# Kernel optimization log

Measured on AMD Instinct MI355X. Metric: run time of the kernel, lower is better.

## Reference

```python
import jax, jax.numpy as jnp
import numpy as np

N_NODES = 100000
N_EDGES = 1600000
IN, HID, OUT = 128, 128, 64


def setup_inputs() -> dict:
    key = jax.random.key(0)
    ks = jax.random.split(key, 12)
    x = jax.random.normal(ks[0], (N_NODES, IN), dtype=jnp.float32)
    src = jax.random.randint(ks[1], (N_EDGES,), 0, N_NODES, dtype=jnp.int32)
    dst = jax.random.randint(ks[2], (N_EDGES,), 0, N_NODES, dtype=jnp.int32)
    def lin(k, fan_in, fan_out):
        s = 1.0 / np.sqrt(fan_in)
        return (jax.random.normal(k, (fan_in, fan_out), dtype=jnp.float32) * s)
    dims = [(IN, HID), (HID, HID), (HID, OUT)]
    params = {}
    for l, (fi, fo) in enumerate(dims):
        params[f"Wself{l}"] = lin(ks[3 + 3 * l], fi, fo)
        params[f"Wneigh{l}"] = lin(ks[4 + 3 * l], fi, fo)
        params[f"b{l}"] = jnp.zeros((fo,), dtype=jnp.float32)
    return {"x": x, "src": src, "dst": dst, **params}


def _sage_conv(h, src, dst, inv_deg, Ws, Wn, b):
    # mean aggregation over in-neighbors: segment-sum of gathered src feats / degree
    agg = jax.ops.segment_sum(h[src], dst, num_segments=N_NODES) * inv_deg
    return h @ Ws + agg @ Wn + b


def reference(x, src, dst, Wself0, Wneigh0, b0, Wself1, Wneigh1, b1, Wself2, Wneigh2, b2):
    deg = jax.ops.segment_sum(jnp.ones((N_EDGES,), jnp.float32), dst, num_segments=N_NODES)
    inv_deg = (1.0 / jnp.maximum(deg, 1.0))[:, None]  # zero-degree nodes get zero agg
    h = jax.nn.relu(_sage_conv(x, src, dst, inv_deg, Wself0, Wneigh0, b0))
    h = jax.nn.relu(_sage_conv(h, src, dst, inv_deg, Wself1, Wneigh1, b1))
    h = _sage_conv(h, src, dst, inv_deg, Wself2, Wneigh2, b2)
    return h
```

## Files before the change

kernel.cpp:

```cpp
#include <hip/hip_runtime.h>
#include <hip/hip_bf16.h>

#define N_NODES 100000
#define N_EDGES 1600000
#define BSHIFT 8
#define NB 391
#define BCAP 8192

typedef __attribute__((ext_vector_type(8))) short short8;
typedef __attribute__((ext_vector_type(4))) float f32x4;
typedef unsigned short ushort;
typedef unsigned int uint;

__device__ __forceinline__ ushort f2bf(float f) {
    uint u = __float_as_uint(f);
    uint r = (u + 0x7fffu + ((u >> 16) & 1u)) >> 16;
    return (ushort)r;
}
__device__ __forceinline__ float bflo(uint v) { return __uint_as_float(v << 16); }
__device__ __forceinline__ float bfhi(uint v) { return __uint_as_float(v & 0xffff0000u); }


__global__ __launch_bounds__(256) void partA_kernel(const int* __restrict__ src,
                                                    const int* __restrict__ dst,
                                                    uint* __restrict__ packed,
                                                    int* __restrict__ bucket_cnt, int E) {
    constexpr int PER = 16;
    __shared__ int cnt[NB];
    __shared__ int cur[NB];
    int tid = threadIdx.x;
    for (int i = tid; i < NB; i += 256) cnt[i] = 0;
    __syncthreads();
    int base = blockIdx.x * (256 * PER);
    int d[PER], s[PER];
#pragma unroll
    for (int i = 0; i < PER; i++) {
        int e = base + tid + i * 256;
        if (e < E) {
            d[i] = dst[e];
            s[i] = src[e];
            atomicAdd(&cnt[d[i] >> BSHIFT], 1);
        } else {
            d[i] = -1;
        }
    }
    __syncthreads();
    for (int i = tid; i < NB; i += 256) cur[i] = atomicAdd(&bucket_cnt[i], cnt[i]);
    __syncthreads();
#pragma unroll
    for (int i = 0; i < PER; i++) {
        if (d[i] >= 0) {
            int b = d[i] >> BSHIFT;
            int p = atomicAdd(&cur[b], 1);
            packed[(size_t)b * BCAP + p] = ((uint)(d[i] & 255) << 17) | (uint)s[i];
        }
    }
}


#define KE 20

__global__ __launch_bounds__(256) void partB_kernel(const uint* __restrict__ packed,
                                                    const int* __restrict__ bucket_cnt,
                                                    int* __restrict__ row_ptr,
                                                    float* __restrict__ inv_deg,
                                                    int* __restrict__ col, int N, int E) {
    __shared__ int deg[256];
    __shared__ int cur[256];
    __shared__ int psum[256];
    __shared__ int sofs;
    int b = blockIdx.x, tid = threadIdx.x;
    int cnt = bucket_cnt[b];
    {
        int part = 0;
        for (int i = tid; i < b; i += 256) part += bucket_cnt[i];
        psum[tid] = part;
        __syncthreads();
        for (int off = 128; off > 0; off >>= 1) {
            if (tid < off) psum[tid] += psum[tid + off];
            __syncthreads();
        }
        if (tid == 0) sofs = psum[0];
        __syncthreads();
    }
    int bofs = sofs;
    const uint* pk = packed + (size_t)b * BCAP;
    deg[tid] = 0;
    __syncthreads();
    uint w[KE];
#pragma unroll
    for (int j = 0; j < KE; j++) {
        int ee = tid + j * 256;
        if (ee < cnt) {
            w[j] = pk[ee];
            atomicAdd(&deg[w[j] >> 17], 1);
        }
    }
    for (int ee = tid + KE * 256; ee < cnt; ee += 256)
        atomicAdd(&deg[pk[ee] >> 17], 1);
    __syncthreads();
    int d0 = deg[tid];
    psum[tid] = d0;
    __syncthreads();
    for (int off = 1; off < 256; off <<= 1) {
        int x = psum[tid];
        int y = (tid >= off) ? psum[tid - off] : 0;
        __syncthreads();
        psum[tid] = x + y;
        __syncthreads();
    }
    int excl = psum[tid] - d0;
    cur[tid] = excl;
    int g = (b << BSHIFT) + tid;
    if (g < N) {
        row_ptr[g] = bofs + excl;
        inv_deg[g] = 1.0f / (float)(d0 > 1 ? d0 : 1);
    }
    if (b == 0 && tid == 0) row_ptr[N] = E;
    __syncthreads();
#pragma unroll
    for (int j = 0; j < KE; j++) {
        int ee = tid + j * 256;
        if (ee < cnt) {
            int p = atomicAdd(&cur[w[j] >> 17], 1);
            col[bofs + p] = (int)(w[j] & 0x1FFFFu);
        }
    }
    for (int ee = tid + KE * 256; ee < cnt; ee += 256) {
        uint ww = pk[ee];
        int p = atomicAdd(&cur[ww >> 17], 1);
        col[bofs + p] = (int)(ww & 0x1FFFFu);
    }
}


#define CAST_BLK 6250

__global__ __launch_bounds__(256) void prep_kernel(const float* __restrict__ x,
                                                   ushort* __restrict__ xb,
                                                   const float* __restrict__ Ws0,
                                                   const float* __restrict__ Wn0,
                                                   const float* __restrict__ Ws1,
                                                   const float* __restrict__ Wn1,
                                                   const float* __restrict__ Ws2,
                                                   const float* __restrict__ Wn2,
                                                   ushort* __restrict__ BT0,
                                                   ushort* __restrict__ BT1,
                                                   ushort* __restrict__ BT2) {
    int blk = blockIdx.x;
    if (blk < CAST_BLK) {
        long n8 = (long)N_NODES * 128 / 8;
        long g = (long)blk * 256 + threadIdx.x;
        if (g >= n8) return;
        const float4* x4 = (const float4*)x;
        float4 a = x4[g * 2], b = x4[g * 2 + 1];
        uint4 o;
        o.x = (uint)f2bf(a.x) | ((uint)f2bf(a.y) << 16);
        o.y = (uint)f2bf(a.z) | ((uint)f2bf(a.w) << 16);
        o.z = (uint)f2bf(b.x) | ((uint)f2bf(b.y) << 16);
        o.w = (uint)f2bf(b.z) | ((uint)f2bf(b.w) << 16);
        ((uint4*)xb)[g] = o;
        return;
    }
    int idx = (blk - CAST_BLK) * 256 + threadIdx.x;
    const float* Ws;
    const float* Wn;
    ushort* BT;
    int FOUT;
    if (idx < 128 * 256) {
        Ws = Ws0; Wn = Wn0; BT = BT0; FOUT = 128;
    } else if (idx < 2 * 128 * 256) {
        idx -= 128 * 256;
        Ws = Ws1; Wn = Wn1; BT = BT1; FOUT = 128;
    } else if (idx < 2 * 128 * 256 + 64 * 256) {
        idx -= 2 * 128 * 256;
        Ws = Ws2; Wn = Wn2; BT = BT2; FOUT = 64;
    } else {
        return;
    }
    int n = idx >> 8, k = idx & 255;
    float v = (k < 128) ? Ws[k * FOUT + n] : Wn[(k - 128) * FOUT + n];
    BT[idx] = f2bf(v);
}


#define ASTR 136

template <int FOUT, bool RELU, bool OUTBF16>
__global__ __launch_bounds__(256) void fused_layer(const ushort* __restrict__ hb,
                                                   const int* __restrict__ row_ptr,
                                                   const int* __restrict__ col,
                                                   const float* __restrict__ inv_deg,
                                                   const ushort* __restrict__ BTb,
                                                   const float* __restrict__ bias,
                                                   void* __restrict__ outp, int nNodes) {
    constexpr int NT = FOUT / 16;
    constexpr int BSTR = 40;
    __shared__ ushort BT[FOUT * BSTR];
    __shared__ ushort AGG[64 * ASTR];
    int tid = threadIdx.x;
    int wave = tid >> 6, lane = tid & 63;
    int quad = lane >> 4, sub = lane & 15;
    int suboff = sub * 16;
    const char* hbase = (const char*)hb;
    int r0 = blockIdx.x * 64 + wave * 16;

    for (int i = 0; i < 16; i++) {
        int node = r0 + i;
        if (node >= nNodes) node = nNodes - 1;
        int beg = row_ptr[node], end = row_ptr[node + 1];
        float acc[8];
#pragma unroll
        for (int j = 0; j < 8; j++) acc[j] = 0.f;
        for (int e0 = beg; e0 < end; e0 += 16) {
            int rem = end - e0;
            int idxv[4];
            float msk[4];
#pragma unroll
            for (int j = 0; j < 4; j++) {
                int ii = quad + 4 * j;
                msk[j] = (ii < rem) ? 1.f : 0.f;
                idxv[j] = col[e0 + ((ii < rem) ? ii : 0)];
            }
            uint4 v[4];
#pragma unroll
            for (int j = 0; j < 4; j++)
                v[j] = *(const uint4*)(hbase + (((uint)idxv[j] << 8) + suboff));
#pragma unroll
            for (int j = 0; j < 4; j++) {
                acc[0] += bflo(v[j].x) * msk[j]; acc[1] += bfhi(v[j].x) * msk[j];
                acc[2] += bflo(v[j].y) * msk[j]; acc[3] += bfhi(v[j].y) * msk[j];
                acc[4] += bflo(v[j].z) * msk[j]; acc[5] += bfhi(v[j].z) * msk[j];
                acc[6] += bflo(v[j].w) * msk[j]; acc[7] += bfhi(v[j].w) * msk[j];
            }
        }
#pragma unroll
        for (int j = 0; j < 8; j++) {
            acc[j] += __shfl_xor(acc[j], 16);
            acc[j] += __shfl_xor(acc[j], 32);
        }
        if (quad == 0) {
            float inv = inv_deg[node];
            uint4 o;
            o.x = (uint)f2bf(acc[0] * inv) | ((uint)f2bf(acc[1] * inv) << 16);
            o.y = (uint)f2bf(acc[2] * inv) | ((uint)f2bf(acc[3] * inv) << 16);
            o.z = (uint)f2bf(acc[4] * inv) | ((uint)f2bf(acc[5] * inv) << 16);
            o.w = (uint)f2bf(acc[6] * inv) | ((uint)f2bf(acc[7] * inv) << 16);
            *(uint4*)&AGG[(wave * 16 + i) * ASTR + sub * 8] = o;
        }
    }
    __syncthreads();

    int m = lane & 15;
    int arow = r0 + m;
    if (arow >= nNodes) arow = nNodes - 1;
    const ushort* hrow = hb + (size_t)arow * 128;

    f32x4 acc[NT];
#pragma unroll
    for (int t = 0; t < NT; t++) acc[t] = (f32x4){0.f, 0.f, 0.f, 0.f};

#pragma unroll
    for (int kc = 0; kc < 8; kc++) {
        __syncthreads();
        constexpr int UNITS = FOUT * 4;
#pragma unroll
        for (int u0 = 0; u0 < UNITS / 256; u0++) {
            int u = tid + u0 * 256;
            int n = u >> 2, ko = (u & 3) * 8;
            short8 v = *(const short8*)(BTb + n * 256 + kc * 32 + ko);
            *(short8*)(&BT[n * BSTR + ko]) = v;
        }
        __syncthreads();
        short8 afrag;
        if (kc < 4) {
            afrag = *(const short8*)(hrow + kc * 32 + quad * 8);
        } else {
            afrag = *(const short8*)(&AGG[(wave * 16 + m) * ASTR + (kc - 4) * 32 + quad * 8]);
        }
#pragma unroll
        for (int t = 0; t < NT; t++) {
            short8 bfrag = *(const short8*)(&BT[(t * 16 + m) * BSTR + quad * 8]);
            acc[t] = __builtin_amdgcn_mfma_f32_16x16x32_bf16(afrag, bfrag, acc[t], 0, 0, 0);
        }
    }

#pragma unroll
    for (int reg = 0; reg < 4; reg++) {
        int orow = r0 + quad * 4 + reg;
        if (orow < nNodes) {
#pragma unroll
            for (int t = 0; t < NT; t++) {
                int j = t * 16 + m;
                float v = acc[t][reg] + bias[j];
                if (RELU) v = fmaxf(v, 0.f);
                if (OUTBF16)
                    ((ushort*)outp)[(size_t)orow * FOUT + j] = f2bf(v);
                else
                    ((float*)outp)[(size_t)orow * FOUT + j] = v;
            }
        }
    }
}

extern "C" void kernel_launch(void* const* d_in, const int* in_sizes, int n_in,
                              void* d_out, int out_size, void* d_ws, size_t ws_size,
                              hipStream_t stream) {
    const float* x   = (const float*)d_in[0];
    const int* src   = (const int*)d_in[1];
    const int* dst   = (const int*)d_in[2];
    const float* Ws0 = (const float*)d_in[3];
    const float* Wn0 = (const float*)d_in[4];
    const float* b0  = (const float*)d_in[5];
    const float* Ws1 = (const float*)d_in[6];
    const float* Wn1 = (const float*)d_in[7];
    const float* b1  = (const float*)d_in[8];
    const float* Ws2 = (const float*)d_in[9];
    const float* Wn2 = (const float*)d_in[10];
    const float* b2  = (const float*)d_in[11];
    float* out = (float*)d_out;

    const int N = N_NODES, E = N_EDGES;

    char* p = (char*)d_ws;
    auto take = [&](size_t bytes) {
        void* r = (void*)p;
        p += (bytes + 255) & ~(size_t)255;
        return r;
    };
    uint* packed    = (uint*)take((size_t)NB * BCAP * 4);
    int* bucket_cnt = (int*)take((size_t)NB * 4);
    int* row_ptr    = (int*)take((size_t)(N + 1) * 4);
    int* col        = (int*)take((size_t)E * 4);
    float* inv_deg  = (float*)take((size_t)N * 4);
    ushort* xb      = (ushort*)take((size_t)N * 128 * 2);
    ushort* h1b     = (ushort*)take((size_t)N * 128 * 2);
    ushort* BT0     = (ushort*)take((size_t)128 * 256 * 2);
    ushort* BT1     = (ushort*)take((size_t)128 * 256 * 2);
    ushort* BT2     = (ushort*)take((size_t)64 * 256 * 2);

    hipMemsetAsync(bucket_cnt, 0, (size_t)NB * 4, stream);
    int nblkA = (E + 4096 - 1) / 4096;
    partA_kernel<<<nblkA, 256, 0, stream>>>(src, dst, packed, bucket_cnt, E);
    partB_kernel<<<NB, 256, 0, stream>>>(packed, bucket_cnt, row_ptr, inv_deg, col, N, E);

    prep_kernel<<<CAST_BLK + 320, 256, 0, stream>>>(x, xb, Ws0, Wn0, Ws1, Wn1, Ws2, Wn2,
                                                    BT0, BT1, BT2);

    int grid = (N + 63) / 64;

    fused_layer<128, true, true><<<grid, 256, 0, stream>>>(xb, row_ptr, col, inv_deg,
                                                           BT0, b0, h1b, N);
    fused_layer<128, true, true><<<grid, 256, 0, stream>>>(h1b, row_ptr, col, inv_deg,
                                                           BT1, b1, xb, N);
    fused_layer<64, false, false><<<grid, 256, 0, stream>>>(xb, row_ptr, col, inv_deg,
                                                            BT2, b2, out, N);
}
```

Before: 420.4 us.

## Split aggregation from GEMM, transform-then-aggregate last layer, fuse prep with partition

The fused per-layer kernel is split into a one-node-per-wave aggregation kernel and a separate MFMA GEMM that computes 32 rows per wave. The last layer now applies the weights before aggregating, so it gathers 64-wide projected features instead of 128-wide inputs. Edge partitioning, input casting and weight transposition are merged into one launch, and partitioning uses per-wave shared counters to reduce atomic contention. In exchange, the aggregated features make an extra round trip through global memory, and there are more kernel launches.

```diff
diff --git a/kernel.cpp b/kernel.cpp
--- a/kernel.cpp
+++ b/kernel.cpp
@@ -21,39 +21,95 @@
 __device__ __forceinline__ float bfhi(uint v) { return __uint_as_float(v & 0xffff0000u); }
 
 
-__global__ __launch_bounds__(256) void partA_kernel(const int* __restrict__ src,
-                                                    const int* __restrict__ dst,
-                                                    uint* __restrict__ packed,
-                                                    int* __restrict__ bucket_cnt, int E) {
-    constexpr int PER = 16;
-    __shared__ int cnt[NB];
-    __shared__ int cur[NB];
+#define CAST_BLK 6250
+#define PREP_BLK (CAST_BLK + 128 + 128 + 64)
+
+__global__ __launch_bounds__(256) void fusedA_kernel(const int* __restrict__ src,
+                                                     const int* __restrict__ dst,
+                                                     uint* __restrict__ packed,
+                                                     int* __restrict__ bucket_cnt, int E,
+                                                     const float* __restrict__ x,
+                                                     ushort* __restrict__ xb,
+                                                     const float* __restrict__ Ws0,
+                                                     const float* __restrict__ Wn0,
+                                                     const float* __restrict__ Ws1,
+                                                     const float* __restrict__ Wn1,
+                                                     const float* __restrict__ Ws2,
+                                                     const float* __restrict__ Wn2,
+                                                     ushort* __restrict__ BT0,
+                                                     ushort* __restrict__ BT1,
+                                                     ushort* __restrict__ BT2) {
+    __shared__ int cnt4[4][NB];
+    __shared__ int cur4[4][NB];
     int tid = threadIdx.x;
-    for (int i = tid; i < NB; i += 256) cnt[i] = 0;
-    __syncthreads();
-    int base = blockIdx.x * (256 * PER);
-    int d[PER], s[PER];
-#pragma unroll
-    for (int i = 0; i < PER; i++) {
-        int e = base + tid + i * 256;
-        if (e < E) {
-            d[i] = dst[e];
-            s[i] = src[e];
-            atomicAdd(&cnt[d[i] >> BSHIFT], 1);
-        } else {
-            d[i] = -1;
-        }
-    }
-    __syncthreads();
-    for (int i = tid; i < NB; i += 256) cur[i] = atomicAdd(&bucket_cnt[i], cnt[i]);
-    __syncthreads();
-#pragma unroll
-    for (int i = 0; i < PER; i++) {
-        if (d[i] >= 0) {
-            int b = d[i] >> BSHIFT;
-            int p = atomicAdd(&cur[b], 1);
-            packed[(size_t)b * BCAP + p] = ((uint)(d[i] & 255) << 17) | (uint)s[i];
-        }
+    if (blockIdx.x < NB) {
+        constexpr int PER = 16;
+        int w = tid >> 6;
+        for (int i = tid; i < 4 * NB; i += 256) ((int*)cnt4)[i] = 0;
+        __syncthreads();
+        int base = blockIdx.x * (256 * PER);
+        int d[PER], s[PER];
+#pragma unroll
+        for (int i = 0; i < PER; i++) {
+            int e = base + tid + i * 256;
+            if (e < E) {
+                d[i] = dst[e];
+                s[i] = src[e];
+                atomicAdd(&cnt4[w][d[i] >> BSHIFT], 1);
+            } else {
+                d[i] = -1;
+            }
+        }
+        __syncthreads();
+        for (int i = tid; i < NB; i += 256) {
+            int c0 = cnt4[0][i], c1 = cnt4[1][i], c2 = cnt4[2][i], c3 = cnt4[3][i];
+            int b0 = atomicAdd(&bucket_cnt[i], c0 + c1 + c2 + c3);
+            cur4[0][i] = b0;
+            cur4[1][i] = b0 + c0;
+            cur4[2][i] = b0 + c0 + c1;
+            cur4[3][i] = b0 + c0 + c1 + c2;
+        }
+        __syncthreads();
+#pragma unroll
+        for (int i = 0; i < PER; i++) {
+            if (d[i] >= 0) {
+                int b = d[i] >> BSHIFT;
+                int p = atomicAdd(&cur4[w][b], 1);
+                packed[(size_t)b * BCAP + p] = ((uint)(d[i] & 255) << 17) | (uint)s[i];
+            }
+        }
+        return;
+    }
+    int blk = blockIdx.x - NB;
+    if (blk < CAST_BLK) {
+        long n8 = (long)N_NODES * 128 / 8;
+        long g = (long)blk * 256 + tid;
+        if (g >= n8) return;
+        const float4* x4 = (const float4*)x;
+        float4 a = x4[g * 2], b = x4[g * 2 + 1];
+        uint4 o;
+        o.x = (uint)f2bf(a.x) | ((uint)f2bf(a.y) << 16);
+        o.y = (uint)f2bf(a.z) | ((uint)f2bf(a.w) << 16);
+        o.z = (uint)f2bf(b.x) | ((uint)f2bf(b.y) << 16);
+        o.w = (uint)f2bf(b.z) | ((uint)f2bf(b.w) << 16);
+        ((uint4*)xb)[g] = o;
+        return;
+    }
+    int idx = (blk - CAST_BLK) * 256 + tid;
+    if (idx < 128 * 256) {
+        int n = idx >> 8, k = idx & 255;
+        float v = (k < 128) ? Ws0[k * 128 + n] : Wn0[(k - 128) * 128 + n];
+        BT0[idx] = f2bf(v);
+    } else if (idx < 2 * 128 * 256) {
+        idx -= 128 * 256;
+        int n = idx >> 8, k = idx & 255;
+        float v = (k < 128) ? Ws1[k * 128 + n] : Wn1[(k - 128) * 128 + n];
+        BT1[idx] = f2bf(v);
+    } else if (idx < 2 * 128 * 256 + 128 * 128) {
+        idx -= 2 * 128 * 256;
+        int n = idx >> 7, k = idx & 127;
+        float v = (n < 64) ? Ws2[k * 64 + n] : Wn2[k * 64 + (n - 64)];
+        BT2[idx] = f2bf(v);
     }
 }
 
@@ -134,131 +190,86 @@
 }
 
 
-#define CAST_BLK 6250
-
-__global__ __launch_bounds__(256) void prep_kernel(const float* __restrict__ x,
-                                                   ushort* __restrict__ xb,
-                                                   const float* __restrict__ Ws0,
-                                                   const float* __restrict__ Wn0,
-                                                   const float* __restrict__ Ws1,
-                                                   const float* __restrict__ Wn1,
-                                                   const float* __restrict__ Ws2,
-                                                   const float* __restrict__ Wn2,
-                                                   ushort* __restrict__ BT0,
-                                                   ushort* __restrict__ BT1,
-                                                   ushort* __restrict__ BT2) {
-    int blk = blockIdx.x;
-    if (blk < CAST_BLK) {
-        long n8 = (long)N_NODES * 128 / 8;
-        long g = (long)blk * 256 + threadIdx.x;
-        if (g >= n8) return;
-        const float4* x4 = (const float4*)x;
-        float4 a = x4[g * 2], b = x4[g * 2 + 1];
+__global__ __launch_bounds__(256) void agg_kernel(const ushort* __restrict__ hb,
+                                                  const int* __restrict__ row_ptr,
+                                                  const int* __restrict__ col,
+                                                  const float* __restrict__ inv_deg,
+                                                  ushort* __restrict__ aggb, int n) {
+    int node = (int)((blockIdx.x * blockDim.x + threadIdx.x) >> 6);
+    int lane = threadIdx.x & 63;
+    if (node >= n) return;
+    int quad = lane >> 4;
+    int sub = lane & 15;
+    const char* hbase = (const char*)hb;
+    int beg = row_ptr[node], end = row_ptr[node + 1];
+    float acc[8];
+#pragma unroll
+    for (int j = 0; j < 8; j++) acc[j] = 0.f;
+    int suboff = sub * 16;
+    for (int e0 = beg; e0 < end; e0 += 16) {
+        int rem = end - e0;
+        int idxv[4];
+        float msk[4];
+#pragma unroll
+        for (int j = 0; j < 4; j++) {
+            int i = quad + 4 * j;
+            msk[j] = (i < rem) ? 1.f : 0.f;
+            idxv[j] = col[e0 + ((i < rem) ? i : 0)];
+        }
+        uint4 v[4];
+#pragma unroll
+        for (int j = 0; j < 4; j++)
+            v[j] = *(const uint4*)(hbase + (((uint)idxv[j] << 8) + suboff));
+#pragma unroll
+        for (int j = 0; j < 4; j++) {
+            acc[0] += bflo(v[j].x) * msk[j]; acc[1] += bfhi(v[j].x) * msk[j];
+            acc[2] += bflo(v[j].y) * msk[j]; acc[3] += bfhi(v[j].y) * msk[j];
+            acc[4] += bflo(v[j].z) * msk[j]; acc[5] += bfhi(v[j].z) * msk[j];
+            acc[6] += bflo(v[j].w) * msk[j]; acc[7] += bfhi(v[j].w) * msk[j];
+        }
+    }
+#pragma unroll
+    for (int j = 0; j < 8; j++) {
+        acc[j] += __shfl_xor(acc[j], 16);
+        acc[j] += __shfl_xor(acc[j], 32);
+    }
+    if (quad == 0) {
+        float inv = inv_deg[node];
         uint4 o;
-        o.x = (uint)f2bf(a.x) | ((uint)f2bf(a.y) << 16);
-        o.y = (uint)f2bf(a.z) | ((uint)f2bf(a.w) << 16);
-        o.z = (uint)f2bf(b.x) | ((uint)f2bf(b.y) << 16);
-        o.w = (uint)f2bf(b.z) | ((uint)f2bf(b.w) << 16);
-        ((uint4*)xb)[g] = o;
-        return;
-    }
-    int idx = (blk - CAST_BLK) * 256 + threadIdx.x;
-    const float* Ws;
-    const float* Wn;
-    ushort* BT;
-    int FOUT;
-    if (idx < 128 * 256) {
-        Ws = Ws0; Wn = Wn0; BT = BT0; FOUT = 128;
-    } else if (idx < 2 * 128 * 256) {
-        idx -= 128 * 256;
-        Ws = Ws1; Wn = Wn1; BT = BT1; FOUT = 128;
-    } else if (idx < 2 * 128 * 256 + 64 * 256) {
-        idx -= 2 * 128 * 256;
-        Ws = Ws2; Wn = Wn2; BT = BT2; FOUT = 64;
-    } else {
-        return;
-    }
-    int n = idx >> 8, k = idx & 255;
-    float v = (k < 128) ? Ws[k * FOUT + n] : Wn[(k - 128) * FOUT + n];
-    BT[idx] = f2bf(v);
-}
-
-
-#define ASTR 136
-
-template <int FOUT, bool RELU, bool OUTBF16>
-__global__ __launch_bounds__(256) void fused_layer(const ushort* __restrict__ hb,
-                                                   const int* __restrict__ row_ptr,
-                                                   const int* __restrict__ col,
-                                                   const float* __restrict__ inv_deg,
-                                                   const ushort* __restrict__ BTb,
-                                                   const float* __restrict__ bias,
-                                                   void* __restrict__ outp, int nNodes) {
+        o.x = (uint)f2bf(acc[0] * inv) | ((uint)f2bf(acc[1] * inv) << 16);
+        o.y = (uint)f2bf(acc[2] * inv) | ((uint)f2bf(acc[3] * inv) << 16);
+        o.z = (uint)f2bf(acc[4] * inv) | ((uint)f2bf(acc[5] * inv) << 16);
+        o.w = (uint)f2bf(acc[6] * inv) | ((uint)f2bf(acc[7] * inv) << 16);
+        *(uint4*)((char*)aggb + (size_t)node * 256 + suboff) = o;
+    }
+}
+
+
+template <int FOUT, bool RELU>
+__global__ __launch_bounds__(256) void mfma_gemm(const ushort* __restrict__ hb,
+                                                 const ushort* __restrict__ aggb,
+                                                 const ushort* __restrict__ BTb,
+                                                 const float* __restrict__ bias,
+                                                 ushort* __restrict__ outp, int nNodes) {
     constexpr int NT = FOUT / 16;
     constexpr int BSTR = 40;
     __shared__ ushort BT[FOUT * BSTR];
-    __shared__ ushort AGG[64 * ASTR];
     int tid = threadIdx.x;
     int wave = tid >> 6, lane = tid & 63;
-    int quad = lane >> 4, sub = lane & 15;
-    int suboff = sub * 16;
-    const char* hbase = (const char*)hb;
-    int r0 = blockIdx.x * 64 + wave * 16;
-
-    for (int i = 0; i < 16; i++) {
-        int node = r0 + i;
-        if (node >= nNodes) node = nNodes - 1;
-        int beg = row_ptr[node], end = row_ptr[node + 1];
-        float acc[8];
-#pragma unroll
-        for (int j = 0; j < 8; j++) acc[j] = 0.f;
-        for (int e0 = beg; e0 < end; e0 += 16) {
-            int rem = end - e0;
-            int idxv[4];
-            float msk[4];
-#pragma unroll
-            for (int j = 0; j < 4; j++) {
-                int ii = quad + 4 * j;
-                msk[j] = (ii < rem) ? 1.f : 0.f;
-                idxv[j] = col[e0 + ((ii < rem) ? ii : 0)];
-            }
-            uint4 v[4];
-#pragma unroll
-            for (int j = 0; j < 4; j++)
-                v[j] = *(const uint4*)(hbase + (((uint)idxv[j] << 8) + suboff));
-#pragma unroll
-            for (int j = 0; j < 4; j++) {
-                acc[0] += bflo(v[j].x) * msk[j]; acc[1] += bfhi(v[j].x) * msk[j];
-                acc[2] += bflo(v[j].y) * msk[j]; acc[3] += bfhi(v[j].y) * msk[j];
-                acc[4] += bflo(v[j].z) * msk[j]; acc[5] += bfhi(v[j].z) * msk[j];
-                acc[6] += bflo(v[j].w) * msk[j]; acc[7] += bfhi(v[j].w) * msk[j];
-            }
-        }
-#pragma unroll
-        for (int j = 0; j < 8; j++) {
-            acc[j] += __shfl_xor(acc[j], 16);
-            acc[j] += __shfl_xor(acc[j], 32);
-        }
-        if (quad == 0) {
-            float inv = inv_deg[node];
-            uint4 o;
-            o.x = (uint)f2bf(acc[0] * inv) | ((uint)f2bf(acc[1] * inv) << 16);
-            o.y = (uint)f2bf(acc[2] * inv) | ((uint)f2bf(acc[3] * inv) << 16);
-            o.z = (uint)f2bf(acc[4] * inv) | ((uint)f2bf(acc[5] * inv) << 16);
-            o.w = (uint)f2bf(acc[6] * inv) | ((uint)f2bf(acc[7] * inv) << 16);
-            *(uint4*)&AGG[(wave * 16 + i) * ASTR + sub * 8] = o;
-        }
-    }
-    __syncthreads();
-
-    int m = lane & 15;
-    int arow = r0 + m;
-    if (arow >= nNodes) arow = nNodes - 1;
-    const ushort* hrow = hb + (size_t)arow * 128;
-
-    f32x4 acc[NT];
-#pragma unroll
-    for (int t = 0; t < NT; t++) acc[t] = (f32x4){0.f, 0.f, 0.f, 0.f};
+    int m = lane & 15, quad = lane >> 4;
+    int r0 = blockIdx.x * 128 + wave * 32;
+    int arow0 = r0 + m;       if (arow0 >= nNodes) arow0 = nNodes - 1;
+    int arow1 = r0 + 16 + m;  if (arow1 >= nNodes) arow1 = nNodes - 1;
+    const ushort* hrow0 = hb + (size_t)arow0 * 128;
+    const ushort* grow0 = aggb + (size_t)arow0 * 128;
+    const ushort* hrow1 = hb + (size_t)arow1 * 128;
+    const ushort* grow1 = aggb + (size_t)arow1 * 128;
+
+    f32x4 acc[2][NT];
+#pragma unroll
+    for (int h = 0; h < 2; h++)
+#pragma unroll
+        for (int t = 0; t < NT; t++) acc[h][t] = (f32x4){0.f, 0.f, 0.f, 0.f};
 
 #pragma unroll
     for (int kc = 0; kc < 8; kc++) {
@@ -272,34 +283,159 @@
             *(short8*)(&BT[n * BSTR + ko]) = v;
         }
         __syncthreads();
-        short8 afrag;
-        if (kc < 4) {
-            afrag = *(const short8*)(hrow + kc * 32 + quad * 8);
-        } else {
-            afrag = *(const short8*)(&AGG[(wave * 16 + m) * ASTR + (kc - 4) * 32 + quad * 8]);
-        }
+        int kg = kc * 32 + quad * 8;
+        const ushort* ap0 = (kg < 128) ? (hrow0 + kg) : (grow0 + (kg - 128));
+        const ushort* ap1 = (kg < 128) ? (hrow1 + kg) : (grow1 + (kg - 128));
+        short8 af0 = *(const short8*)ap0;
+        short8 af1 = *(const short8*)ap1;
 #pragma unroll
         for (int t = 0; t < NT; t++) {
             short8 bfrag = *(const short8*)(&BT[(t * 16 + m) * BSTR + quad * 8]);
-            acc[t] = __builtin_amdgcn_mfma_f32_16x16x32_bf16(afrag, bfrag, acc[t], 0, 0, 0);
-        }
-    }
-
-#pragma unroll
-    for (int reg = 0; reg < 4; reg++) {
-        int orow = r0 + quad * 4 + reg;
-        if (orow < nNodes) {
-#pragma unroll
-            for (int t = 0; t < NT; t++) {
-                int j = t * 16 + m;
-                float v = acc[t][reg] + bias[j];
-                if (RELU) v = fmaxf(v, 0.f);
-                if (OUTBF16)
-                    ((ushort*)outp)[(size_t)orow * FOUT + j] = f2bf(v);
-                else
-                    ((float*)outp)[(size_t)orow * FOUT + j] = v;
+            acc[0][t] = __builtin_amdgcn_mfma_f32_16x16x32_bf16(af0, bfrag, acc[0][t], 0, 0, 0);
+            acc[1][t] = __builtin_amdgcn_mfma_f32_16x16x32_bf16(af1, bfrag, acc[1][t], 0, 0, 0);
+        }
+    }
+
+#pragma unroll
+    for (int h = 0; h < 2; h++)
+#pragma unroll
+        for (int reg = 0; reg < 4; reg++) {
+            int orow = r0 + h * 16 + quad * 4 + reg;
+            if (orow < nNodes) {
+#pragma unroll
+                for (int t = 0; t < NT; t++) {
+                    int j = t * 16 + m;
+                    float v = acc[h][t][reg] + bias[j];
+                    if (RELU) v = fmaxf(v, 0.f);
+                    outp[(size_t)orow * FOUT + j] = f2bf(v);
+                }
             }
         }
+}
+
+
+__global__ __launch_bounds__(256) void gemm2a_kernel(const ushort* __restrict__ hb,
+                                                     const ushort* __restrict__ BT2b,
+                                                     const float* __restrict__ bias,
+                                                     float* __restrict__ zs,
+                                                     ushort* __restrict__ y2, int nNodes) {
+    constexpr int NT = 8;
+    constexpr int BSTR = 40;
+    __shared__ ushort BT[128 * BSTR];
+    int tid = threadIdx.x;
+    int wave = tid >> 6, lane = tid & 63;
+    int m = lane & 15, quad = lane >> 4;
+    int r0 = blockIdx.x * 128 + wave * 32;
+    int arow0 = r0 + m;       if (arow0 >= nNodes) arow0 = nNodes - 1;
+    int arow1 = r0 + 16 + m;  if (arow1 >= nNodes) arow1 = nNodes - 1;
+    const ushort* hrow0 = hb + (size_t)arow0 * 128;
+    const ushort* hrow1 = hb + (size_t)arow1 * 128;
+
+    f32x4 acc[2][NT];
+#pragma unroll
+    for (int h = 0; h < 2; h++)
+#pragma unroll
+        for (int t = 0; t < NT; t++) acc[h][t] = (f32x4){0.f, 0.f, 0.f, 0.f};
+
+#pragma unroll
+    for (int kc = 0; kc < 4; kc++) {
+        __syncthreads();
+#pragma unroll
+        for (int u0 = 0; u0 < 2; u0++) {
+            int u = tid + u0 * 256;
+            int n = u >> 2, ko = (u & 3) * 8;
+            short8 v = *(const short8*)(BT2b + n * 128 + kc * 32 + ko);
+            *(short8*)(&BT[n * BSTR + ko]) = v;
+        }
+        __syncthreads();
+        int kg = kc * 32 + quad * 8;
+        short8 af0 = *(const short8*)(hrow0 + kg);
+        short8 af1 = *(const short8*)(hrow1 + kg);
+#pragma unroll
+        for (int t = 0; t < NT; t++) {
+            short8 bfrag = *(const short8*)(&BT[(t * 16 + m) * BSTR + quad * 8]);
+            acc[0][t] = __builtin_amdgcn_mfma_f32_16x16x32_bf16(af0, bfrag, acc[0][t], 0, 0, 0);
+            acc[1][t] = __builtin_amdgcn_mfma_f32_16x16x32_bf16(af1, bfrag, acc[1][t], 0, 0, 0);
+        }
+    }
+
+#pragma unroll
+    for (int h = 0; h < 2; h++)
+#pragma unroll
+        for (int reg = 0; reg < 4; reg++) {
+            int orow = r0 + h * 16 + quad * 4 + reg;
+            if (orow < nNodes) {
+#pragma unroll
+                for (int t = 0; t < 4; t++) {
+                    int j = t * 16 + m;
+                    zs[(size_t)orow * 64 + j] = acc[h][t][reg] + bias[j];
+                }
+#pragma unroll
+                for (int t = 4; t < 8; t++) {
+                    int j = (t - 4) * 16 + m;
+                    y2[(size_t)orow * 64 + j] = f2bf(acc[h][t][reg]);
+                }
+            }
+        }
+}
+
+
+__global__ __launch_bounds__(256) void agg2_kernel(const ushort* __restrict__ y2,
+                                                   const int* __restrict__ row_ptr,
+                                                   const int* __restrict__ col,
+                                                   const float* __restrict__ inv_deg,
+                                                   const float* __restrict__ zs,
+                                                   float* __restrict__ out, int n) {
+    int node = (int)((blockIdx.x * blockDim.x + threadIdx.x) >> 6);
+    int lane = threadIdx.x & 63;
+    if (node >= n) return;
+    int oct = lane >> 3;
+    int sub = lane & 7;
+    const char* ybase = (const char*)y2;
+    int beg = row_ptr[node], end = row_ptr[node + 1];
+    float acc[8];
+#pragma unroll
+    for (int j = 0; j < 8; j++) acc[j] = 0.f;
+    int suboff = sub * 16;
+    for (int e0 = beg; e0 < end; e0 += 16) {
+        int rem = end - e0;
+        int idxv[2];
+        float msk[2];
+#pragma unroll
+        for (int j = 0; j < 2; j++) {
+            int i = oct + 8 * j;
+            msk[j] = (i < rem) ? 1.f : 0.f;
+            idxv[j] = col[e0 + ((i < rem) ? i : 0)];
+        }
+        uint4 v[2];
+#pragma unroll
+        for (int j = 0; j < 2; j++)
+            v[j] = *(const uint4*)(ybase + (((uint)idxv[j] << 7) + suboff));
+#pragma unroll
+        for (int j = 0; j < 2; j++) {
+            acc[0] += bflo(v[j].x) * msk[j]; acc[1] += bfhi(v[j].x) * msk[j];
+            acc[2] += bflo(v[j].y) * msk[j]; acc[3] += bfhi(v[j].y) * msk[j];
+            acc[4] += bflo(v[j].z) * msk[j]; acc[5] += bfhi(v[j].z) * msk[j];
+            acc[6] += bflo(v[j].w) * msk[j]; acc[7] += bfhi(v[j].w) * msk[j];
+        }
+    }
+#pragma unroll
+    for (int j = 0; j < 8; j++) {
+        acc[j] += __shfl_xor(acc[j], 8);
+        acc[j] += __shfl_xor(acc[j], 16);
+        acc[j] += __shfl_xor(acc[j], 32);
+    }
+    if (oct == 0) {
+        float inv = inv_deg[node];
+        const float4* z = (const float4*)(zs + (size_t)node * 64 + sub * 8);
+        float4 z0 = z[0], z1 = z[1];
+        float4 o0, o1;
+        o0.x = z0.x + acc[0] * inv; o0.y = z0.y + acc[1] * inv;
+        o0.z = z0.z + acc[2] * inv; o0.w = z0.w + acc[3] * inv;
+        o1.x = z1.x + acc[4] * inv; o1.y = z1.y + acc[5] * inv;
+        o1.z = z1.z + acc[6] * inv; o1.w = z1.w + acc[7] * inv;
+        float4* op = (float4*)(out + (size_t)node * 64 + sub * 8);
+        op[0] = o0; op[1] = o1;
     }
 }
 
@@ -335,24 +471,26 @@
     float* inv_deg  = (float*)take((size_t)N * 4);
     ushort* xb      = (ushort*)take((size_t)N * 128 * 2);
     ushort* h1b     = (ushort*)take((size_t)N * 128 * 2);
+    ushort* aggb    = (ushort*)take((size_t)N * 128 * 2);
     ushort* BT0     = (ushort*)take((size_t)128 * 256 * 2);
     ushort* BT1     = (ushort*)take((size_t)128 * 256 * 2);
-    ushort* BT2     = (ushort*)take((size_t)64 * 256 * 2);
+    ushort* BT2     = (ushort*)take((size_t)128 * 128 * 2);
+    ushort* y2 = (ushort*)packed;
+    float* zs = (float*)aggb;
 
     hipMemsetAsync(bucket_cnt, 0, (size_t)NB * 4, stream);
-    int nblkA = (E + 4096 - 1) / 4096;
-    partA_kernel<<<nblkA, 256, 0, stream>>>(src, dst, packed, bucket_cnt, E);
+    fusedA_kernel<<<NB + PREP_BLK, 256, 0, stream>>>(src, dst, packed, bucket_cnt, E,
+                                                     x, xb, Ws0, Wn0, Ws1, Wn1, Ws2, Wn2,
+                                                     BT0, BT1, BT2);
     partB_kernel<<<NB, 256, 0, stream>>>(packed, bucket_cnt, row_ptr, inv_deg, col, N, E);
 
-    prep_kernel<<<CAST_BLK + 320, 256, 0, stream>>>(x, xb, Ws0, Wn0, Ws1, Wn1, Ws2, Wn2,
-                                                    BT0, BT1, BT2);
-
-    int grid = (N + 63) / 64;
-
-    fused_layer<128, true, true><<<grid, 256, 0, stream>>>(xb, row_ptr, col, inv_deg,
-                                                           BT0, b0, h1b, N);
-    fused_layer<128, true, true><<<grid, 256, 0, stream>>>(h1b, row_ptr, col, inv_deg,
-                                                           BT1, b1, xb, N);
-    fused_layer<64, false, false><<<grid, 256, 0, stream>>>(xb, row_ptr, col, inv_deg,
-                                                            BT2, b2, out, N);
-}
+    int aggGrid = (int)(((long)N * 64 + 255) / 256);
+    int gemmGrid = (N + 127) / 128;
+
+    agg_kernel<<<aggGrid, 256, 0, stream>>>(xb, row_ptr, col, inv_deg, aggb, N);
+    mfma_gemm<128, true><<<gemmGrid, 256, 0, stream>>>(xb, aggb, BT0, b0, h1b, N);
+    agg_kernel<<<aggGrid, 256, 0, stream>>>(h1b, row_ptr, col, inv_deg, aggb, N);
+    mfma_gemm<128, true><<<gemmGrid, 256, 0, stream>>>(h1b, aggb, BT1, b1, xb, N);
+    gemm2a_kernel<<<gemmGrid, 256, 0, stream>>>(xb, BT2, b2, zs, y2, N);
+    agg2_kernel<<<aggGrid, 256, 0, stream>>>(y2, row_ptr, col, inv_deg, zs, out, N);
+}
```

Measured after the change: 360.9 us. -14.1%, faster.
